# Performance work log

Hardware: AMD Instinct MI355X
Metric: run time of the kernel (lower is better)

Reference implementation:

```python
import jax, jax.numpy as jnp
import numpy as np
from jax import lax

OBS_DIM = 128      # proj_size == obs_dim
HIDDEN = 1024      # cell size
OUT_SAMPLES = 8192 # last 64 timesteps * 128
B, T = 64, 2048


def _lstmp_layer(x, Wih, Whh, bih, bhh, Whr):
    """One LSTM layer with projection (PyTorch proj_size semantics).
    x: [B, T, in]; Wih: [4H, in]; Whh: [4H, P]; Whr: [P, H].
    Gate order i, f, g, o. Returns [B, T, P]."""
    Bv = x.shape[0]
    H = Whh.shape[0] // 4
    P = Whr.shape[0]
    # input contribution for all timesteps in one GEMM: [B, T, 4H]
    xg = jnp.einsum('bti,gi->btg', x, Wih) + bih

    def step(carry, xg_t):
        h, c = carry                       # h: [B,P], c: [B,H]
        g = xg_t + h @ Whh.T + bhh         # [B, 4H]
        i, f, gg, o = jnp.split(g, 4, axis=-1)
        c = jax.nn.sigmoid(f) * c + jax.nn.sigmoid(i) * jnp.tanh(gg)
        h = (jax.nn.sigmoid(o) * jnp.tanh(c)) @ Whr.T  # project to [B,P]
        return (h, c), h

    h0 = jnp.zeros((Bv, P), x.dtype)
    c0 = jnp.zeros((Bv, H), x.dtype)
    (_, _), hs = lax.scan(step, (h0, c0), jnp.swapaxes(xg, 0, 1))
    return jnp.swapaxes(hs, 0, 1)          # [B, T, P]


def setup_inputs() -> dict:
    key = jax.random.key(0)
    ks = jax.random.split(key, 12)
    s = 1.0 / np.sqrt(HIDDEN)
    P, H = OBS_DIM, HIDDEN
    d = {
        'x': jax.random.normal(ks[0], (B, T, OBS_DIM), dtype=jnp.float32),
        # layer 0: input size = obs_dim
        'Wih0': jax.random.uniform(ks[1], (4 * H, OBS_DIM), minval=-s, maxval=s),
        'Whh0': jax.random.uniform(ks[2], (4 * H, P), minval=-s, maxval=s),
        'bih0': jax.random.uniform(ks[3], (4 * H,), minval=-s, maxval=s),
        'bhh0': jax.random.uniform(ks[4], (4 * H,), minval=-s, maxval=s),
        'Whr0': jax.random.uniform(ks[5], (P, H), minval=-s, maxval=s),
        # layer 1: input size = proj_size = obs_dim
        'Wih1': jax.random.uniform(ks[6], (4 * H, P), minval=-s, maxval=s),
        'Whh1': jax.random.uniform(ks[7], (4 * H, P), minval=-s, maxval=s),
        'bih1': jax.random.uniform(ks[8], (4 * H,), minval=-s, maxval=s),
        'bhh1': jax.random.uniform(ks[9], (4 * H,), minval=-s, maxval=s),
        'Whr1': jax.random.uniform(ks[10], (P, H), minval=-s, maxval=s),
    }
    return d


def reference(x, Wih0, Whh0, bih0, bhh0, Whr0, Wih1, Whh1, bih1, bhh1, Whr1):
    xb = x.reshape(x.shape[0], -1, OBS_DIM)
    h1 = _lstmp_layer(xb, Wih0, Whh0, bih0, bhh0, Whr0)
    h2 = _lstmp_layer(h1, Wih1, Whh1, bih1, bhh1, Whr1)
    outs = h2.reshape(h2.shape[0], -1)
    return outs[:, -OUT_SAMPLES:]
```

## Files before the change

### kernel.cpp

```cpp
#include <hip/hip_runtime.h>
#include <hip/hip_fp16.h>


typedef _Float16 f16;
typedef _Float16 f16x4 __attribute__((ext_vector_type(4)));
typedef _Float16 f16x8 __attribute__((ext_vector_type(8)));
typedef float f32x4 __attribute__((ext_vector_type(4)));
typedef unsigned long long u64;
struct U128 { u64 lo, hi; };

#define TSTEPS 2048
#define NW 32
#define TIMEOUT_TICKS 200000000ull

#define BSW_OFF  0ull
#define BSW_SZ   (64ull*32768ull*2ull)
#define WHR_OFF  (BSW_OFF + BSW_SZ)
#define WHR_SZ   (64ull*4096ull*2ull)
#define BIAS_OFF (WHR_OFF + WHR_SZ)
#define BIAS_SZ  (8192ull*4ull)
#define HACC_OFF (BIAS_OFF + BIAS_SZ)
#define HACC_SZ  (2ull*8ull*8192ull*4ull)
#define CNT_OFF  (HACC_OFF + HACC_SZ)
#define CNT_SZ   (256ull)
#define WS_NEED  (CNT_OFF + CNT_SZ)

__device__ __forceinline__ float sigm(float v) {
  float e = __builtin_amdgcn_exp2f(-1.4426950408889634f * v);
  return __builtin_amdgcn_rcpf(1.0f + e);
}
__device__ __forceinline__ float tanh_(float v) {
  float a = fabsf(v);
  float e = __builtin_amdgcn_exp2f(-2.8853900817779268f * a);
  float r = (1.0f - e) * __builtin_amdgcn_rcpf(1.0f + e);
  return copysignf(r, v);
}

__device__ __forceinline__ u64 ald64(const void* p) {
  return __hip_atomic_load((const u64*)p, __ATOMIC_RELAXED, __HIP_MEMORY_SCOPE_AGENT);
}
__device__ __forceinline__ unsigned ald32u(const unsigned* p) {
  return __hip_atomic_load(p, __ATOMIC_RELAXED, __HIP_MEMORY_SCOPE_AGENT);
}
__device__ __forceinline__ void ast32f(float* p, float v) {
  __hip_atomic_store((unsigned*)p, __builtin_bit_cast(unsigned, v),
                     __ATOMIC_RELAXED, __HIP_MEMORY_SCOPE_AGENT);
}
__device__ __forceinline__ void ast32u(unsigned* p, unsigned v) {
  __hip_atomic_store(p, v, __ATOMIC_RELAXED, __HIP_MEMORY_SCOPE_AGENT);
}
__device__ __forceinline__ f32x4 ald_f32x4(const float* p) {
  U128 u; u.lo = ald64(p); u.hi = ald64(p + 2);
  return __builtin_bit_cast(f32x4, u);
}
__device__ __forceinline__ void aadd_f32(float* p, float v) {
  (void)__hip_atomic_fetch_add(p, v, __ATOMIC_RELAXED, __HIP_MEMORY_SCOPE_AGENT);
}
__device__ __forceinline__ void vm_drain() {
  asm volatile("s_waitcnt vmcnt(0)" ::: "memory");
}

__global__ void lstm_setup(
    const float* __restrict__ Wih0, const float* __restrict__ Whh0,
    const float* __restrict__ bih0, const float* __restrict__ bhh0,
    const float* __restrict__ Whr0,
    const float* __restrict__ Wih1, const float* __restrict__ Whh1,
    const float* __restrict__ bih1, const float* __restrict__ bhh1,
    const float* __restrict__ Whr1,
    f16* __restrict__ Bsw, f16* __restrict__ Whrsw, float* __restrict__ bias,
    float* __restrict__ hacc, unsigned* __restrict__ cnt)
{
  const int blk = blockIdx.x, tid = threadIdx.x;
  if (blk < 64) {
    const int lyr = blk >> 5, w = blk & 31;
    const float* Whh = lyr ? Whh1 : Whh0;
    const float* Wih = lyr ? Wih1 : Wih0;
    f16* dst = Bsw + (size_t)blk * 32768;
    for (int e = tid; e < 32768; e += 256) {
      int i = e & 7, l = (e >> 3) & 63, ntG = (e >> 9) & 7, ks = e >> 12;
      int k  = ks * 32 + (l >> 4) * 8 + i;
      int rl = ntG * 16 + (l & 15);
      int grow = (rl >> 5) * 1024 + w * 32 + (rl & 31);
      float v = (k < 128) ? Whh[grow * 128 + k] : Wih[grow * 128 + (k - 128)];
      dst[e] = (f16)v;
    }
  } else if (blk < 128) {
    const int q = blk - 64, lyr = q >> 5, w = q & 31;
    const float* Whr = lyr ? Whr1 : Whr0;
    f16* dst = Whrsw + (size_t)q * 4096;
    for (int e = tid; e < 4096; e += 256) {
      int i = e & 7, l = (e >> 3) & 63, pnG = e >> 9;
      int p = pnG * 16 + (l & 15);
      int hg = w * 32 + (l >> 4) * 8 + i;
      dst[e] = (f16)Whr[p * 1024 + hg];
    }
  } else if (blk == 128) {
    for (int e = tid; e < 8192; e += 256) {
      int lyr = e >> 12, j = e & 4095;
      bias[e] = lyr ? (bih1[j] + bhh1[j]) : (bih0[j] + bhh0[j]);
    }
  } else {
    for (int e = tid; e < 2 * 8 * 8192; e += 256) ast32f(hacc + e, 0.f);
    if (tid < 64) ast32u(cnt + tid, 0u);
  }
}

__global__ __launch_bounds__(256, 1) void lstm_main(
    const float* __restrict__ x, float* __restrict__ out,
    const f16* __restrict__ Bsw, const f16* __restrict__ Whrsw,
    const float* __restrict__ bias, float* __restrict__ hacc,
    unsigned* __restrict__ cnt)
{
  const int tid = threadIdx.x;
  const int lane = tid & 63, wv = tid >> 6;
  const int wy = wv >> 1, wx = wv & 1;
  const int l15 = lane & 15, lg = lane >> 4;
  const int w = blockIdx.x & 31, lyr = blockIdx.x >> 5;

  const u64 tstart = __builtin_amdgcn_s_memrealtime();
  bool tmo = false;

  __shared__ __align__(16) f16 h_lds[64][136];
  __shared__ __align__(16) f16 x1_lds[64][136];
  __shared__ __align__(16) f16 s_lds[64][40];
  __shared__ int s_go;
  if (tid == 0) s_go = 0;

  f16x8 bf[8][4];
  {
    const f16* bsl = Bsw + (size_t)(lyr * NW + w) * 32768;
#pragma unroll
    for (int ks = 0; ks < 8; ++ks)
#pragma unroll
      for (int ntl = 0; ntl < 4; ++ntl)
        bf[ks][ntl] = *(const f16x8*)(bsl + (((ks * 8 + (ntl * 2 + wx)) * 64 + lane) * 8));
  }
  f16x8 wf[4];
  {
    const f16* wsl = Whrsw + (size_t)(lyr * NW + w) * 4096;
#pragma unroll
    for (int pnl = 0; pnl < 4; ++pnl)
      wf[pnl] = *(const f16x8*)(wsl + (((pnl * 2 + wx) * 64 + lane) * 8));
  }
  float bias_r[4];
#pragma unroll
  for (int ntl = 0; ntl < 4; ++ntl)
    bias_r[ntl] = bias[lyr * 4096 + ntl * 1024 + w * 32 + wx * 16 + l15];

  float c[2][4] = {{0.f,0.f,0.f,0.f},{0.f,0.f,0.f,0.f}};

  float* myacc = hacc + (size_t)lyr * 8 * 8192;
  float* h1a   = hacc;
  unsigned* c0 = cnt;
  unsigned* c1 = cnt + 1;
  __syncthreads();

  for (int t = 0; t <= TSTEPS; ++t) {
    if (lyr == 0 && t == TSTEPS) break;
    const bool tail = (t == TSTEPS);

    f16x8 xr[2][4];
    if (lyr == 0) {
#pragma unroll
      for (int mtl = 0; mtl < 2; ++mtl) {
        const int bbx = (wy * 2 + mtl) * 16 + l15;
        const float* xp = x + ((size_t)bbx * TSTEPS + t) * 128 + lg * 8;
#pragma unroll
        for (int ks2 = 0; ks2 < 4; ++ks2) {
          f32x4 v0 = *(const f32x4*)(xp + ks2 * 32);
          f32x4 v1 = *(const f32x4*)(xp + ks2 * 32 + 4);
          f16x8 hx;
          hx[0]=(f16)v0[0]; hx[1]=(f16)v0[1]; hx[2]=(f16)v0[2]; hx[3]=(f16)v0[3];
          hx[4]=(f16)v1[0]; hx[5]=(f16)v1[1]; hx[6]=(f16)v1[2]; hx[7]=(f16)v1[3];
          xr[mtl][ks2] = hx;
        }
      }
    }

    if (wv == 0) {
      for (;;) {
        bool ok = true;
        if (lane == 0) {
          ok = ald32u(lyr ? c1 : c0) >= (unsigned)(32 * t);
        } else if (lane == 1) {
          if (lyr == 0) ok = (t < 4) || (ald32u(c1) >= (unsigned)(32 * (t - 3)));
          else          ok = tail || (ald32u(c0) >= (unsigned)(32 * (t + 1)));
        }
        if ((__builtin_amdgcn_s_memrealtime() - tstart) > TIMEOUT_TICKS) { ok = true; tmo = true; }
        if (__all(ok)) break;
        __builtin_amdgcn_s_sleep(1);
      }
      __atomic_store_n(&s_go, t + 1, __ATOMIC_RELAXED);
    } else {
      while (__atomic_load_n(&s_go, __ATOMIC_RELAXED) < t + 1)
        __builtin_amdgcn_s_sleep(1);
    }
    asm volatile("" ::: "memory");

    {
      const int b = tid >> 2, pb = (tid & 3) * 32;
      const float* hp = myacc + (size_t)((t + 7) & 7) * 8192 + b * 128 + pb;
      f32x4 hv4[8];
#pragma unroll
      for (int k = 0; k < 8; ++k) hv4[k] = ald_f32x4(hp + k * 4);
      if (lyr == 1 && t >= TSTEPS - 63 && (tid & 3) == (w >> 3))
        *(f32x4*)(out + (size_t)b * 8192 + (t - 1 - (TSTEPS - 64)) * 128 + w * 4) = hv4[w & 7];
#pragma unroll
      for (int k = 0; k < 8; ++k) {
        f16x4 h16;
#pragma unroll
        for (int e = 0; e < 4; ++e) h16[e] = (f16)hv4[k][e];
        *(f16x4*)(&h_lds[b][pb + k * 4]) = h16;
      }
      if (lyr == 1 && !tail) {
        const float* xp1 = h1a + (size_t)(t & 7) * 8192 + b * 128 + pb;
#pragma unroll
        for (int k = 0; k < 8; ++k) {
          f32x4 v = ald_f32x4(xp1 + k * 4);
          f16x4 h16;
#pragma unroll
          for (int e = 0; e < 4; ++e) h16[e] = (f16)v[e];
          *(f16x4*)(&x1_lds[b][pb + k * 4]) = h16;
        }
      }
      if (!tail)
        ast32f(myacc + (size_t)((t + 4) & 7) * 8192 + b * 128 + w * 4 + (tid & 3), 0.f);
    }
    if (tail) break;
    __syncthreads();

#pragma unroll
    for (int mtl = 0; mtl < 2; ++mtl) {
      f16x8 af[8];
#pragma unroll
      for (int ks = 0; ks < 4; ++ks)
        af[ks] = *(const f16x8*)(&h_lds[(wy * 2 + mtl) * 16 + l15][ks * 32 + lg * 8]);
      if (lyr == 0) {
        af[4] = xr[mtl][0]; af[5] = xr[mtl][1];
        af[6] = xr[mtl][2]; af[7] = xr[mtl][3];
      } else {
#pragma unroll
        for (int ks2 = 0; ks2 < 4; ++ks2)
          af[4 + ks2] = *(const f16x8*)(&x1_lds[(wy * 2 + mtl) * 16 + l15][ks2 * 32 + lg * 8]);
      }
      f32x4 acc[4];
#pragma unroll
      for (int ntl = 0; ntl < 4; ++ntl) {
        f32x4 b4 = {bias_r[ntl], bias_r[ntl], bias_r[ntl], bias_r[ntl]};
        acc[ntl] = b4;
      }
#pragma unroll
      for (int ks = 0; ks < 8; ++ks)
#pragma unroll
        for (int ntl = 0; ntl < 4; ++ntl)
          acc[ntl] = __builtin_amdgcn_mfma_f32_16x16x32_f16(af[ks], bf[ks][ntl], acc[ntl], 0, 0, 0);
#pragma unroll
      for (int r = 0; r < 4; ++r) {
        float gi = acc[0][r], gf = acc[1][r], gg = acc[2][r], go = acc[3][r];
        float cc = sigm(gf) * c[mtl][r] + sigm(gi) * tanh_(gg);
        c[mtl][r] = cc;
        float s = sigm(go) * tanh_(cc);
        s_lds[(wy * 2 + mtl) * 16 + lg * 4 + r][wx * 16 + l15] = (f16)s;
      }
    }
    __syncthreads();

    {
      float* dst = myacc + (size_t)(t & 7) * 8192;
#pragma unroll
      for (int pml = 0; pml < 2; ++pml) {
        f16x8 ap = *(const f16x8*)(&s_lds[(wy * 2 + pml) * 16 + l15][lg * 8]);
#pragma unroll
        for (int pnl = 0; pnl < 4; ++pnl) {
          f32x4 z = {0.f, 0.f, 0.f, 0.f};
          f32x4 pa = __builtin_amdgcn_mfma_f32_16x16x32_f16(ap, wf[pnl], z, 0, 0, 0);
          const int p = (pnl * 2 + wx) * 16 + l15;
#pragma unroll
          for (int r = 0; r < 4; ++r) {
            const int b = (wy * 2 + pml) * 16 + lg * 4 + r;
            aadd_f32(dst + b * 128 + p, pa[r]);
          }
        }
      }
    }
    vm_drain();
    __syncthreads();
    if (tid == 0)
      (void)__hip_atomic_fetch_add(lyr ? c1 : c0, 1u, __ATOMIC_RELAXED, __HIP_MEMORY_SCOPE_AGENT);
  }

  if (tmo && tid == 0) out[0] = 12345.0f;
}

extern "C" void kernel_launch(void* const* d_in, const int* in_sizes, int n_in,
                              void* d_out, int out_size, void* d_ws, size_t ws_size,
                              hipStream_t stream)
{
  const float* x    = (const float*)d_in[0];
  const float* Wih0 = (const float*)d_in[1];
  const float* Whh0 = (const float*)d_in[2];
  const float* bih0 = (const float*)d_in[3];
  const float* bhh0 = (const float*)d_in[4];
  const float* Whr0 = (const float*)d_in[5];
  const float* Wih1 = (const float*)d_in[6];
  const float* Whh1 = (const float*)d_in[7];
  const float* bih1 = (const float*)d_in[8];
  const float* bhh1 = (const float*)d_in[9];
  const float* Whr1 = (const float*)d_in[10];

  if (ws_size < WS_NEED) return;

  char* ws = (char*)d_ws;
  f16*      Bsw   = (f16*)(ws + BSW_OFF);
  f16*      Whrsw = (f16*)(ws + WHR_OFF);
  float*    bias  = (float*)(ws + BIAS_OFF);
  float*    hacc  = (float*)(ws + HACC_OFF);
  unsigned* cnt   = (unsigned*)(ws + CNT_OFF);

  lstm_setup<<<130, 256, 0, stream>>>(Wih0, Whh0, bih0, bhh0, Whr0,
                                      Wih1, Whh1, bih1, bhh1, Whr1,
                                      Bsw, Whrsw, bias, hacc, cnt);
  lstm_main<<<64, 256, 0, stream>>>(x, (float*)d_out, Bsw, Whrsw, bias,
                                    hacc, cnt);
}
```

Baseline: 17.88 ms.

## Halve persistent workgroups per layer and replace shared counters with per-WG step flags

Reduces the persistent grid from 32 to 16 workgroups per layer, each owning 64 hidden units, with every wave covering all 64 batch rows and one 16-unit slice per gate. The weight swizzle and projection K-split are reworked to match. The layer-0 input MFMA is issued before the barrier wait so it overlaps the spin, and the single atomic counter per layer becomes 16 per-workgroup step flags polled by separate lanes. Fewer workgroups means fewer atomic-add contributors and cheaper inter-WG synchronisation, at the cost of twice the MFMA and elementwise work per workgroup on the serial critical path.

```diff
diff --git a/kernel.cpp b/kernel.cpp
--- a/kernel.cpp
+++ b/kernel.cpp
@@ -10,20 +10,20 @@
 struct U128 { u64 lo, hi; };
 
 #define TSTEPS 2048
-#define NW 32
+#define NWG 16
 #define TIMEOUT_TICKS 200000000ull
 
 #define BSW_OFF  0ull
-#define BSW_SZ   (64ull*32768ull*2ull)
+#define BSW_SZ   (32ull*65536ull*2ull)
 #define WHR_OFF  (BSW_OFF + BSW_SZ)
-#define WHR_SZ   (64ull*4096ull*2ull)
+#define WHR_SZ   (32ull*8192ull*2ull)
 #define BIAS_OFF (WHR_OFF + WHR_SZ)
-#define BIAS_SZ  (8192ull*4ull)
+#define BIAS_SZ  (2ull*16ull*256ull*4ull)
 #define HACC_OFF (BIAS_OFF + BIAS_SZ)
 #define HACC_SZ  (2ull*8ull*8192ull*4ull)
-#define CNT_OFF  (HACC_OFF + HACC_SZ)
-#define CNT_SZ   (256ull)
-#define WS_NEED  (CNT_OFF + CNT_SZ)
+#define FLAG_OFF (HACC_OFF + HACC_SZ)
+#define FLAG_SZ  (256ull)
+#define WS_NEED  (FLAG_OFF + FLAG_SZ)
 
 __device__ __forceinline__ float sigm(float v) {
   float e = __builtin_amdgcn_exp2f(-1.4426950408889634f * v);
@@ -68,40 +68,41 @@
     const float* __restrict__ bih1, const float* __restrict__ bhh1,
     const float* __restrict__ Whr1,
     f16* __restrict__ Bsw, f16* __restrict__ Whrsw, float* __restrict__ bias,
-    float* __restrict__ hacc, unsigned* __restrict__ cnt)
+    float* __restrict__ hacc, unsigned* __restrict__ flags)
 {
   const int blk = blockIdx.x, tid = threadIdx.x;
-  if (blk < 64) {
-    const int lyr = blk >> 5, w = blk & 31;
+  if (blk < 32) {
+    const int lyr = blk >> 4, w = blk & 15;
     const float* Whh = lyr ? Whh1 : Whh0;
     const float* Wih = lyr ? Wih1 : Wih0;
-    f16* dst = Bsw + (size_t)blk * 32768;
-    for (int e = tid; e < 32768; e += 256) {
-      int i = e & 7, l = (e >> 3) & 63, ntG = (e >> 9) & 7, ks = e >> 12;
-      int k  = ks * 32 + (l >> 4) * 8 + i;
-      int rl = ntG * 16 + (l & 15);
-      int grow = (rl >> 5) * 1024 + w * 32 + (rl & 31);
+    f16* dst = Bsw + (size_t)blk * 65536;
+    for (int e = tid; e < 65536; e += 256) {
+      int i = e & 7, l = (e >> 3) & 63, n = (e >> 9) & 15, ks = e >> 13;
+      int k    = ks * 32 + (l >> 4) * 8 + i;
+      int gate = n >> 2, u = (n & 3) * 16 + (l & 15);
+      int grow = gate * 1024 + w * 64 + u;
       float v = (k < 128) ? Whh[grow * 128 + k] : Wih[grow * 128 + (k - 128)];
       dst[e] = (f16)v;
     }
-  } else if (blk < 128) {
-    const int q = blk - 64, lyr = q >> 5, w = q & 31;
+  } else if (blk < 64) {
+    const int q = blk - 32, lyr = q >> 4, w = q & 15;
     const float* Whr = lyr ? Whr1 : Whr0;
-    f16* dst = Whrsw + (size_t)q * 4096;
-    for (int e = tid; e < 4096; e += 256) {
-      int i = e & 7, l = (e >> 3) & 63, pnG = e >> 9;
-      int p = pnG * 16 + (l & 15);
-      int hg = w * 32 + (l >> 4) * 8 + i;
-      dst[e] = (f16)Whr[p * 1024 + hg];
-    }
-  } else if (blk == 128) {
+    f16* dst = Whrsw + (size_t)q * 8192;
     for (int e = tid; e < 8192; e += 256) {
-      int lyr = e >> 12, j = e & 4095;
-      bias[e] = lyr ? (bih1[j] + bhh1[j]) : (bih0[j] + bhh0[j]);
+      int i = e & 7, l = (e >> 3) & 63, ks2 = (e >> 9) & 1, pt = e >> 10;
+      int p  = pt * 16 + (l & 15);
+      int kl = ks2 * 32 + (l >> 4) * 8 + i;
+      dst[e] = (f16)Whr[p * 1024 + w * 64 + kl];
+    }
+  } else if (blk == 64) {
+    for (int e = tid; e < 8192; e += 256) {
+      int lyr = e >> 12, w = (e >> 8) & 15, rl = e & 255;
+      int grow = (rl >> 6) * 1024 + w * 64 + (rl & 63);
+      bias[e] = lyr ? (bih1[grow] + bhh1[grow]) : (bih0[grow] + bhh0[grow]);
     }
   } else {
     for (int e = tid; e < 2 * 8 * 8192; e += 256) ast32f(hacc + e, 0.f);
-    if (tid < 64) ast32u(cnt + tid, 0u);
+    if (tid < 32) ast32u(flags + tid, 0u);
   }
 }
 
@@ -109,62 +110,69 @@
     const float* __restrict__ x, float* __restrict__ out,
     const f16* __restrict__ Bsw, const f16* __restrict__ Whrsw,
     const float* __restrict__ bias, float* __restrict__ hacc,
-    unsigned* __restrict__ cnt)
+    unsigned* __restrict__ flags)
 {
   const int tid = threadIdx.x;
   const int lane = tid & 63, wv = tid >> 6;
-  const int wy = wv >> 1, wx = wv & 1;
   const int l15 = lane & 15, lg = lane >> 4;
-  const int w = blockIdx.x & 31, lyr = blockIdx.x >> 5;
+  const int w = blockIdx.x & 15, lyr = blockIdx.x >> 4;
 
   const u64 tstart = __builtin_amdgcn_s_memrealtime();
   bool tmo = false;
 
   __shared__ __align__(16) f16 h_lds[64][136];
   __shared__ __align__(16) f16 x1_lds[64][136];
-  __shared__ __align__(16) f16 s_lds[64][40];
+  __shared__ __align__(16) f16 s_lds[64][72];
   __shared__ int s_go;
   if (tid == 0) s_go = 0;
 
   f16x8 bf[8][4];
   {
-    const f16* bsl = Bsw + (size_t)(lyr * NW + w) * 32768;
+    const f16* bsl = Bsw + (size_t)(lyr * NWG + w) * 65536;
 #pragma unroll
     for (int ks = 0; ks < 8; ++ks)
 #pragma unroll
-      for (int ntl = 0; ntl < 4; ++ntl)
-        bf[ks][ntl] = *(const f16x8*)(bsl + (((ks * 8 + (ntl * 2 + wx)) * 64 + lane) * 8));
+      for (int g = 0; g < 4; ++g)
+        bf[ks][g] = *(const f16x8*)(bsl + (((ks * 16 + g * 4 + wv) * 64 + lane) * 8));
   }
-  f16x8 wf[4];
+  f16x8 wf[2][2];
   {
-    const f16* wsl = Whrsw + (size_t)(lyr * NW + w) * 4096;
-#pragma unroll
-    for (int pnl = 0; pnl < 4; ++pnl)
-      wf[pnl] = *(const f16x8*)(wsl + (((pnl * 2 + wx) * 64 + lane) * 8));
+    const f16* wsl = Whrsw + (size_t)(lyr * NWG + w) * 8192;
+#pragma unroll
+    for (int pt = 0; pt < 2; ++pt)
+#pragma unroll
+      for (int ks2 = 0; ks2 < 2; ++ks2)
+        wf[pt][ks2] = *(const f16x8*)(wsl + ((((wv + pt * 4) * 2 + ks2) * 64 + lane) * 8));
   }
   float bias_r[4];
 #pragma unroll
-  for (int ntl = 0; ntl < 4; ++ntl)
-    bias_r[ntl] = bias[lyr * 4096 + ntl * 1024 + w * 32 + wx * 16 + l15];
-
-  float c[2][4] = {{0.f,0.f,0.f,0.f},{0.f,0.f,0.f,0.f}};
-
+  for (int g = 0; g < 4; ++g)
+    bias_r[g] = bias[(lyr * 16 + w) * 256 + g * 64 + wv * 16 + l15];
+
+  float c[4][4] = {{0,0,0,0},{0,0,0,0},{0,0,0,0},{0,0,0,0}};
+
+  unsigned* f0 = flags;
+  unsigned* f1 = flags + 16;
   float* myacc = hacc + (size_t)lyr * 8 * 8192;
   float* h1a   = hacc;
-  unsigned* c0 = cnt;
-  unsigned* c1 = cnt + 1;
   __syncthreads();
 
   for (int t = 0; t <= TSTEPS; ++t) {
     if (lyr == 0 && t == TSTEPS) break;
     const bool tail = (t == TSTEPS);
 
-    f16x8 xr[2][4];
+    f32x4 acc[4][4];
+#pragma unroll
+    for (int mtl = 0; mtl < 4; ++mtl)
+#pragma unroll
+      for (int g = 0; g < 4; ++g) {
+        f32x4 b4 = {bias_r[g], bias_r[g], bias_r[g], bias_r[g]};
+        acc[mtl][g] = b4;
+      }
     if (lyr == 0) {
 #pragma unroll
-      for (int mtl = 0; mtl < 2; ++mtl) {
-        const int bbx = (wy * 2 + mtl) * 16 + l15;
-        const float* xp = x + ((size_t)bbx * TSTEPS + t) * 128 + lg * 8;
+      for (int mtl = 0; mtl < 4; ++mtl) {
+        const float* xp = x + ((size_t)(mtl * 16 + l15) * TSTEPS + t) * 128 + lg * 8;
 #pragma unroll
         for (int ks2 = 0; ks2 < 4; ++ks2) {
           f32x4 v0 = *(const f32x4*)(xp + ks2 * 32);
@@ -172,7 +180,9 @@
           f16x8 hx;
           hx[0]=(f16)v0[0]; hx[1]=(f16)v0[1]; hx[2]=(f16)v0[2]; hx[3]=(f16)v0[3];
           hx[4]=(f16)v1[0]; hx[5]=(f16)v1[1]; hx[6]=(f16)v1[2]; hx[7]=(f16)v1[3];
-          xr[mtl][ks2] = hx;
+#pragma unroll
+          for (int g = 0; g < 4; ++g)
+            acc[mtl][g] = __builtin_amdgcn_mfma_f32_16x16x32_f16(hx, bf[4 + ks2][g], acc[mtl][g], 0, 0, 0);
         }
       }
     }
@@ -180,11 +190,11 @@
     if (wv == 0) {
       for (;;) {
         bool ok = true;
-        if (lane == 0) {
-          ok = ald32u(lyr ? c1 : c0) >= (unsigned)(32 * t);
-        } else if (lane == 1) {
-          if (lyr == 0) ok = (t < 4) || (ald32u(c1) >= (unsigned)(32 * (t - 3)));
-          else          ok = tail || (ald32u(c0) >= (unsigned)(32 * (t + 1)));
+        if (lane < 16) {
+          ok = ald32u((lyr ? f1 : f0) + lane) >= (unsigned)t;
+        } else if (lane < 32) {
+          if (lyr == 0) ok = (t < 4) || (ald32u(f1 + lane - 16) >= (unsigned)(t - 3));
+          else          ok = tail || (ald32u(f0 + lane - 16) >= (unsigned)(t + 1));
         }
         if ((__builtin_amdgcn_s_memrealtime() - tstart) > TIMEOUT_TICKS) { ok = true; tmo = true; }
         if (__all(ok)) break;
@@ -203,8 +213,12 @@
       f32x4 hv4[8];
 #pragma unroll
       for (int k = 0; k < 8; ++k) hv4[k] = ald_f32x4(hp + k * 4);
-      if (lyr == 1 && t >= TSTEPS - 63 && (tid & 3) == (w >> 3))
-        *(f32x4*)(out + (size_t)b * 8192 + (t - 1 - (TSTEPS - 64)) * 128 + w * 4) = hv4[w & 7];
+      if (lyr == 1 && t >= TSTEPS - 63 && (tid & 3) == (w >> 2)) {
+        const int k0 = (w & 3) * 2;
+        float* op = out + (size_t)b * 8192 + (t - 1 - (TSTEPS - 64)) * 128 + 8 * w;
+        *(f32x4*)op = hv4[k0];
+        *(f32x4*)(op + 4) = hv4[k0 + 1];
+      }
 #pragma unroll
       for (int k = 0; k < 8; ++k) {
         f16x4 h16;
@@ -223,44 +237,41 @@
           *(f16x4*)(&x1_lds[b][pb + k * 4]) = h16;
         }
       }
-      if (!tail)
-        ast32f(myacc + (size_t)((t + 4) & 7) * 8192 + b * 128 + w * 4 + (tid & 3), 0.f);
+      if (!tail) {
+        float* z = myacc + (size_t)((t + 4) & 7) * 8192 + b * 128 + 8 * w + (tid & 3) * 2;
+        ast32f(z, 0.f);
+        ast32f(z + 1, 0.f);
+      }
     }
     if (tail) break;
     __syncthreads();
 
 #pragma unroll
-    for (int mtl = 0; mtl < 2; ++mtl) {
-      f16x8 af[8];
-#pragma unroll
-      for (int ks = 0; ks < 4; ++ks)
-        af[ks] = *(const f16x8*)(&h_lds[(wy * 2 + mtl) * 16 + l15][ks * 32 + lg * 8]);
-      if (lyr == 0) {
-        af[4] = xr[mtl][0]; af[5] = xr[mtl][1];
-        af[6] = xr[mtl][2]; af[7] = xr[mtl][3];
-      } else {
-#pragma unroll
-        for (int ks2 = 0; ks2 < 4; ++ks2)
-          af[4 + ks2] = *(const f16x8*)(&x1_lds[(wy * 2 + mtl) * 16 + l15][ks2 * 32 + lg * 8]);
-      }
-      f32x4 acc[4];
-#pragma unroll
-      for (int ntl = 0; ntl < 4; ++ntl) {
-        f32x4 b4 = {bias_r[ntl], bias_r[ntl], bias_r[ntl], bias_r[ntl]};
-        acc[ntl] = b4;
-      }
-#pragma unroll
-      for (int ks = 0; ks < 8; ++ks)
-#pragma unroll
-        for (int ntl = 0; ntl < 4; ++ntl)
-          acc[ntl] = __builtin_amdgcn_mfma_f32_16x16x32_f16(af[ks], bf[ks][ntl], acc[ntl], 0, 0, 0);
+    for (int mtl = 0; mtl < 4; ++mtl) {
+#pragma unroll
+      for (int ks = 0; ks < 4; ++ks) {
+        f16x8 af = *(const f16x8*)(&h_lds[mtl * 16 + l15][ks * 32 + lg * 8]);
+#pragma unroll
+        for (int g = 0; g < 4; ++g)
+          acc[mtl][g] = __builtin_amdgcn_mfma_f32_16x16x32_f16(af, bf[ks][g], acc[mtl][g], 0, 0, 0);
+      }
+      if (lyr == 1) {
+#pragma unroll
+        for (int ks2 = 0; ks2 < 4; ++ks2) {
+          f16x8 xf = *(const f16x8*)(&x1_lds[mtl * 16 + l15][ks2 * 32 + lg * 8]);
+#pragma unroll
+          for (int g = 0; g < 4; ++g)
+            acc[mtl][g] = __builtin_amdgcn_mfma_f32_16x16x32_f16(xf, bf[4 + ks2][g], acc[mtl][g], 0, 0, 0);
+        }
+      }
 #pragma unroll
       for (int r = 0; r < 4; ++r) {
-        float gi = acc[0][r], gf = acc[1][r], gg = acc[2][r], go = acc[3][r];
+        float gi = acc[mtl][0][r], gf = acc[mtl][1][r];
+        float gg = acc[mtl][2][r], go = acc[mtl][3][r];
         float cc = sigm(gf) * c[mtl][r] + sigm(gi) * tanh_(gg);
         c[mtl][r] = cc;
         float s = sigm(go) * tanh_(cc);
-        s_lds[(wy * 2 + mtl) * 16 + lg * 4 + r][wx * 16 + l15] = (f16)s;
+        s_lds[mtl * 16 + lg * 4 + r][wv * 16 + l15] = (f16)s;
       }
     }
     __syncthreads();
@@ -268,25 +279,24 @@
     {
       float* dst = myacc + (size_t)(t & 7) * 8192;
 #pragma unroll
-      for (int pml = 0; pml < 2; ++pml) {
-        f16x8 ap = *(const f16x8*)(&s_lds[(wy * 2 + pml) * 16 + l15][lg * 8]);
-#pragma unroll
-        for (int pnl = 0; pnl < 4; ++pnl) {
+      for (int mtl = 0; mtl < 4; ++mtl) {
+        f16x8 ap0 = *(const f16x8*)(&s_lds[mtl * 16 + l15][lg * 8]);
+        f16x8 ap1 = *(const f16x8*)(&s_lds[mtl * 16 + l15][32 + lg * 8]);
+#pragma unroll
+        for (int pt = 0; pt < 2; ++pt) {
           f32x4 z = {0.f, 0.f, 0.f, 0.f};
-          f32x4 pa = __builtin_amdgcn_mfma_f32_16x16x32_f16(ap, wf[pnl], z, 0, 0, 0);
-          const int p = (pnl * 2 + wx) * 16 + l15;
-#pragma unroll
-          for (int r = 0; r < 4; ++r) {
-            const int b = (wy * 2 + pml) * 16 + lg * 4 + r;
-            aadd_f32(dst + b * 128 + p, pa[r]);
-          }
+          f32x4 pa = __builtin_amdgcn_mfma_f32_16x16x32_f16(ap0, wf[pt][0], z, 0, 0, 0);
+          pa = __builtin_amdgcn_mfma_f32_16x16x32_f16(ap1, wf[pt][1], pa, 0, 0, 0);
+          const int p = (wv + pt * 4) * 16 + l15;
+#pragma unroll
+          for (int r = 0; r < 4; ++r)
+            aadd_f32(dst + (mtl * 16 + lg * 4 + r) * 128 + p, pa[r]);
         }
       }
     }
     vm_drain();
     __syncthreads();
-    if (tid == 0)
-      (void)__hip_atomic_fetch_add(lyr ? c1 : c0, 1u, __ATOMIC_RELAXED, __HIP_MEMORY_SCOPE_AGENT);
+    if (tid == 0) ast32u((lyr ? f1 : f0) + w, (unsigned)(t + 1));
   }
 
   if (tmo && tid == 0) out[0] = 12345.0f;
@@ -315,11 +325,11 @@
   f16*      Whrsw = (f16*)(ws + WHR_OFF);
   float*    bias  = (float*)(ws + BIAS_OFF);
   float*    hacc  = (float*)(ws + HACC_OFF);
-  unsigned* cnt   = (unsigned*)(ws + CNT_OFF);
-
-  lstm_setup<<<130, 256, 0, stream>>>(Wih0, Whh0, bih0, bhh0, Whr0,
-                                      Wih1, Whh1, bih1, bhh1, Whr1,
-                                      Bsw, Whrsw, bias, hacc, cnt);
-  lstm_main<<<64, 256, 0, stream>>>(x, (float*)d_out, Bsw, Whrsw, bias,
-                                    hacc, cnt);
-}
+  unsigned* flags = (unsigned*)(ws + FLAG_OFF);
+
+  lstm_setup<<<66, 256, 0, stream>>>(Wih0, Whh0, bih0, bhh0, Whr0,
+                                     Wih1, Whh1, bih1, bhh1, Whr1,
+                                     Bsw, Whrsw, bias, hacc, flags);
+  lstm_main<<<32, 256, 0, stream>>>(x, (float*)d_out, Bsw, Whrsw, bias,
+                                    hacc, flags);
+}
```

After: 22.07 ms. +23.4%, slower.

## Replace shared atomic counters with per-block step flags and hoist input GEMM before wait

Applied to the files above, without the earlier changes.

Replaces the single fetch-add counter per layer with per-block flags that each block stores its step into. Every wave now polls all 32 flags of both layers itself instead of waiting on an LDS broadcast from wave 0. For layer 0 the x-input MFMAs are moved before the spin-wait so they overlap with waiting for other blocks. Layer 1 issues its input loads alongside the h loads. This aims to cut atomic contention and per-step barrier latency, at the cost of more polling traffic from all waves.

```diff
diff --git a/kernel.cpp b/kernel.cpp
--- a/kernel.cpp
+++ b/kernel.cpp
@@ -21,9 +21,9 @@
 #define BIAS_SZ  (8192ull*4ull)
 #define HACC_OFF (BIAS_OFF + BIAS_SZ)
 #define HACC_SZ  (2ull*8ull*8192ull*4ull)
-#define CNT_OFF  (HACC_OFF + HACC_SZ)
-#define CNT_SZ   (256ull)
-#define WS_NEED  (CNT_OFF + CNT_SZ)
+#define FLAG_OFF (HACC_OFF + HACC_SZ)
+#define FLAG_SZ  (512ull)
+#define WS_NEED  (FLAG_OFF + FLAG_SZ)
 
 __device__ __forceinline__ float sigm(float v) {
   float e = __builtin_amdgcn_exp2f(-1.4426950408889634f * v);
@@ -68,7 +68,7 @@
     const float* __restrict__ bih1, const float* __restrict__ bhh1,
     const float* __restrict__ Whr1,
     f16* __restrict__ Bsw, f16* __restrict__ Whrsw, float* __restrict__ bias,
-    float* __restrict__ hacc, unsigned* __restrict__ cnt)
+    float* __restrict__ hacc, unsigned* __restrict__ flags)
 {
   const int blk = blockIdx.x, tid = threadIdx.x;
   if (blk < 64) {
@@ -101,7 +101,7 @@
     }
   } else {
     for (int e = tid; e < 2 * 8 * 8192; e += 256) ast32f(hacc + e, 0.f);
-    if (tid < 64) ast32u(cnt + tid, 0u);
+    if (tid < 128) ast32u(flags + tid, 0u);
   }
 }
 
@@ -109,7 +109,7 @@
     const float* __restrict__ x, float* __restrict__ out,
     const f16* __restrict__ Bsw, const f16* __restrict__ Whrsw,
     const float* __restrict__ bias, float* __restrict__ hacc,
-    unsigned* __restrict__ cnt)
+    unsigned* __restrict__ flags)
 {
   const int tid = threadIdx.x;
   const int lane = tid & 63, wv = tid >> 6;
@@ -123,8 +123,6 @@
   __shared__ __align__(16) f16 h_lds[64][136];
   __shared__ __align__(16) f16 x1_lds[64][136];
   __shared__ __align__(16) f16 s_lds[64][40];
-  __shared__ int s_go;
-  if (tid == 0) s_go = 0;
 
   f16x8 bf[8][4];
   {
@@ -149,22 +147,29 @@
 
   float c[2][4] = {{0.f,0.f,0.f,0.f},{0.f,0.f,0.f,0.f}};
 
+  unsigned* f0 = flags;
+  unsigned* f1 = flags + 32;
+  unsigned* myf = lyr ? f1 : f0;
   float* myacc = hacc + (size_t)lyr * 8 * 8192;
   float* h1a   = hacc;
-  unsigned* c0 = cnt;
-  unsigned* c1 = cnt + 1;
   __syncthreads();
 
   for (int t = 0; t <= TSTEPS; ++t) {
     if (lyr == 0 && t == TSTEPS) break;
     const bool tail = (t == TSTEPS);
 
-    f16x8 xr[2][4];
+    f32x4 acc[2][4];
+#pragma unroll
+    for (int mtl = 0; mtl < 2; ++mtl)
+#pragma unroll
+      for (int ntl = 0; ntl < 4; ++ntl) {
+        f32x4 b4 = {bias_r[ntl], bias_r[ntl], bias_r[ntl], bias_r[ntl]};
+        acc[mtl][ntl] = b4;
+      }
     if (lyr == 0) {
 #pragma unroll
       for (int mtl = 0; mtl < 2; ++mtl) {
-        const int bbx = (wy * 2 + mtl) * 16 + l15;
-        const float* xp = x + ((size_t)bbx * TSTEPS + t) * 128 + lg * 8;
+        const float* xp = x + ((size_t)((wy * 2 + mtl) * 16 + l15) * TSTEPS + t) * 128 + lg * 8;
 #pragma unroll
         for (int ks2 = 0; ks2 < 4; ++ks2) {
           f32x4 v0 = *(const f32x4*)(xp + ks2 * 32);
@@ -172,28 +177,25 @@
           f16x8 hx;
           hx[0]=(f16)v0[0]; hx[1]=(f16)v0[1]; hx[2]=(f16)v0[2]; hx[3]=(f16)v0[3];
           hx[4]=(f16)v1[0]; hx[5]=(f16)v1[1]; hx[6]=(f16)v1[2]; hx[7]=(f16)v1[3];
-          xr[mtl][ks2] = hx;
+#pragma unroll
+          for (int ntl = 0; ntl < 4; ++ntl)
+            acc[mtl][ntl] = __builtin_amdgcn_mfma_f32_16x16x32_f16(hx, bf[4 + ks2][ntl], acc[mtl][ntl], 0, 0, 0);
         }
       }
     }
 
-    if (wv == 0) {
-      for (;;) {
-        bool ok = true;
-        if (lane == 0) {
-          ok = ald32u(lyr ? c1 : c0) >= (unsigned)(32 * t);
-        } else if (lane == 1) {
-          if (lyr == 0) ok = (t < 4) || (ald32u(c1) >= (unsigned)(32 * (t - 3)));
-          else          ok = tail || (ald32u(c0) >= (unsigned)(32 * (t + 1)));
-        }
-        if ((__builtin_amdgcn_s_memrealtime() - tstart) > TIMEOUT_TICKS) { ok = true; tmo = true; }
-        if (__all(ok)) break;
-        __builtin_amdgcn_s_sleep(1);
-      }
-      __atomic_store_n(&s_go, t + 1, __ATOMIC_RELAXED);
-    } else {
-      while (__atomic_load_n(&s_go, __ATOMIC_RELAXED) < t + 1)
-        __builtin_amdgcn_s_sleep(1);
+    for (;;) {
+      bool ok = true;
+      if (lane < 32) {
+        ok = ald32u(myf + lane) >= (unsigned)t;
+      } else {
+        const int l2 = lane - 32;
+        if (lyr == 0) ok = (t < 4) || (ald32u(f1 + l2) >= (unsigned)(t - 3));
+        else          ok = tail || (ald32u(f0 + l2) >= (unsigned)(t + 1));
+      }
+      if ((__builtin_amdgcn_s_memrealtime() - tstart) > TIMEOUT_TICKS) { ok = true; tmo = true; }
+      if (__all(ok)) break;
+      __builtin_amdgcn_s_sleep(1);
     }
     asm volatile("" ::: "memory");
 
@@ -203,6 +205,12 @@
       f32x4 hv4[8];
 #pragma unroll
       for (int k = 0; k < 8; ++k) hv4[k] = ald_f32x4(hp + k * 4);
+      f32x4 x1v[8];
+      if (lyr == 1 && !tail) {
+        const float* xp1 = h1a + (size_t)(t & 7) * 8192 + b * 128 + pb;
+#pragma unroll
+        for (int k = 0; k < 8; ++k) x1v[k] = ald_f32x4(xp1 + k * 4);
+      }
       if (lyr == 1 && t >= TSTEPS - 63 && (tid & 3) == (w >> 3))
         *(f32x4*)(out + (size_t)b * 8192 + (t - 1 - (TSTEPS - 64)) * 128 + w * 4) = hv4[w & 7];
 #pragma unroll
@@ -213,13 +221,11 @@
         *(f16x4*)(&h_lds[b][pb + k * 4]) = h16;
       }
       if (lyr == 1 && !tail) {
-        const float* xp1 = h1a + (size_t)(t & 7) * 8192 + b * 128 + pb;
 #pragma unroll
         for (int k = 0; k < 8; ++k) {
-          f32x4 v = ald_f32x4(xp1 + k * 4);
           f16x4 h16;
 #pragma unroll
-          for (int e = 0; e < 4; ++e) h16[e] = (f16)v[e];
+          for (int e = 0; e < 4; ++e) h16[e] = (f16)x1v[k][e];
           *(f16x4*)(&x1_lds[b][pb + k * 4]) = h16;
         }
       }
@@ -231,32 +237,26 @@
 
 #pragma unroll
     for (int mtl = 0; mtl < 2; ++mtl) {
-      f16x8 af[8];
-#pragma unroll
-      for (int ks = 0; ks < 4; ++ks)
-        af[ks] = *(const f16x8*)(&h_lds[(wy * 2 + mtl) * 16 + l15][ks * 32 + lg * 8]);
-      if (lyr == 0) {
-        af[4] = xr[mtl][0]; af[5] = xr[mtl][1];
-        af[6] = xr[mtl][2]; af[7] = xr[mtl][3];
-      } else {
-#pragma unroll
-        for (int ks2 = 0; ks2 < 4; ++ks2)
-          af[4 + ks2] = *(const f16x8*)(&x1_lds[(wy * 2 + mtl) * 16 + l15][ks2 * 32 + lg * 8]);
-      }
-      f32x4 acc[4];
-#pragma unroll
-      for (int ntl = 0; ntl < 4; ++ntl) {
-        f32x4 b4 = {bias_r[ntl], bias_r[ntl], bias_r[ntl], bias_r[ntl]};
-        acc[ntl] = b4;
-      }
-#pragma unroll
-      for (int ks = 0; ks < 8; ++ks)
+#pragma unroll
+      for (int ks = 0; ks < 4; ++ks) {
+        f16x8 af = *(const f16x8*)(&h_lds[(wy * 2 + mtl) * 16 + l15][ks * 32 + lg * 8]);
 #pragma unroll
         for (int ntl = 0; ntl < 4; ++ntl)
-          acc[ntl] = __builtin_amdgcn_mfma_f32_16x16x32_f16(af[ks], bf[ks][ntl], acc[ntl], 0, 0, 0);
+          acc[mtl][ntl] = __builtin_amdgcn_mfma_f32_16x16x32_f16(af, bf[ks][ntl], acc[mtl][ntl], 0, 0, 0);
+      }
+      if (lyr == 1) {
+#pragma unroll
+        for (int ks2 = 0; ks2 < 4; ++ks2) {
+          f16x8 xf = *(const f16x8*)(&x1_lds[(wy * 2 + mtl) * 16 + l15][ks2 * 32 + lg * 8]);
+#pragma unroll
+          for (int ntl = 0; ntl < 4; ++ntl)
+            acc[mtl][ntl] = __builtin_amdgcn_mfma_f32_16x16x32_f16(xf, bf[4 + ks2][ntl], acc[mtl][ntl], 0, 0, 0);
+        }
+      }
 #pragma unroll
       for (int r = 0; r < 4; ++r) {
-        float gi = acc[0][r], gf = acc[1][r], gg = acc[2][r], go = acc[3][r];
+        float gi = acc[mtl][0][r], gf = acc[mtl][1][r];
+        float gg = acc[mtl][2][r], go = acc[mtl][3][r];
         float cc = sigm(gf) * c[mtl][r] + sigm(gi) * tanh_(gg);
         c[mtl][r] = cc;
         float s = sigm(go) * tanh_(cc);
@@ -285,8 +285,7 @@
     }
     vm_drain();
     __syncthreads();
-    if (tid == 0)
-      (void)__hip_atomic_fetch_add(lyr ? c1 : c0, 1u, __ATOMIC_RELAXED, __HIP_MEMORY_SCOPE_AGENT);
+    if (tid == 0) ast32u(myf + w, (unsigned)(t + 1));
   }
 
   if (tmo && tid == 0) out[0] = 12345.0f;
@@ -315,11 +314,11 @@
   f16*      Whrsw = (f16*)(ws + WHR_OFF);
   float*    bias  = (float*)(ws + BIAS_OFF);
   float*    hacc  = (float*)(ws + HACC_OFF);
-  unsigned* cnt   = (unsigned*)(ws + CNT_OFF);
+  unsigned* flags = (unsigned*)(ws + FLAG_OFF);
 
   lstm_setup<<<130, 256, 0, stream>>>(Wih0, Whh0, bih0, bhh0, Whr0,
                                       Wih1, Whh1, bih1, bhh1, Whr1,
-                                      Bsw, Whrsw, bias, hacc, cnt);
+                                      Bsw, Whrsw, bias, hacc, flags);
   lstm_main<<<64, 256, 0, stream>>>(x, (float*)d_out, Bsw, Whrsw, bias,
-                                    hacc, cnt);
-}
+                                    hacc, flags);
+}
```

Result: faster. 17.21 ms (-3.8%).
